# Kernel optimization log

Hardware: AMD Instinct MI355X
Metric: run time of the kernel (lower is better)

Reference implementation:

```python
import jax, jax.numpy as jnp
import numpy as np

N_NODES = 20000
N_EDGES = 320000
N_GRAPHS = 256
HIDDEN = 128
L = 4
NUM_ATOM = 28
NUM_BOND = 4
AVG_LOG = float(np.log(17.0))  # avg degree 16 -> avg_d['log']
EPS = 1e-5


def setup_inputs() -> dict:
    key = jax.random.key(0)
    ks = jax.random.split(key, 16)
    D = HIDDEN
    return {
        "x": jax.random.randint(ks[0], (N_NODES,), 0, NUM_ATOM, dtype=jnp.int32),
        "batch": jnp.sort(jax.random.randint(ks[1], (N_NODES,), 0, N_GRAPHS, dtype=jnp.int32)),
        "edge_index": jax.random.randint(ks[2], (2, N_EDGES), 0, N_NODES, dtype=jnp.int32),
        "snorm_n": jax.random.uniform(ks[3], (N_NODES, 1), dtype=jnp.float32),
        "edge_attr": jax.random.randint(ks[4], (N_EDGES,), 0, NUM_BOND, dtype=jnp.int32),
        "atom_emb": jax.random.normal(ks[5], (NUM_ATOM, D), jnp.float32) * 0.1,
        "bond_emb": jax.random.normal(ks[6], (NUM_BOND, D), jnp.float32) * 0.1,
        "pre_W": jax.random.normal(ks[7], (L, 3 * D, D), jnp.float32) / np.sqrt(3 * D),
        "pre_b": jnp.zeros((L, D), jnp.float32),
        "post_W": jax.random.normal(ks[8], (L, 13 * D, D), jnp.float32) / np.sqrt(13 * D),
        "post_b": jnp.zeros((L, D), jnp.float32),
        "mix_W": jax.random.normal(ks[9], (L, D, D), jnp.float32) / np.sqrt(D),
        "mix_b": jnp.zeros((L, D), jnp.float32),
        "bn_gamma": jnp.ones((L, D), jnp.float32),
        "bn_beta": jnp.zeros((L, D), jnp.float32),
        "r_W1": jax.random.normal(ks[10], (D, D // 2), jnp.float32) / np.sqrt(D),
        "r_b1": jnp.zeros((D // 2,), jnp.float32),
        "r_W2": jax.random.normal(ks[11], (D // 2, D // 4), jnp.float32) / np.sqrt(D // 2),
        "r_b2": jnp.zeros((D // 4,), jnp.float32),
        "r_W3": jax.random.normal(ks[12], (D // 4, 1), jnp.float32) / np.sqrt(D // 4),
        "r_b3": jnp.zeros((1,), jnp.float32),
    }


def _pna_forward(x, batch, edge_index, snorm_n, edge_attr,
                 atom_emb, bond_emb, pre_W, pre_b, post_W, post_b,
                 mix_W, mix_b, bn_gamma, bn_beta,
                 r_W1, r_b1, r_W2, r_b2, r_W3, r_b3):
    src, dst = edge_index[0], edge_index[1]
    h = atom_emb[x]                          # [N, D]
    e = bond_emb[edge_attr]                  # [E, D]
    # in-degree and PNA degree scalers (computed once)
    d = jax.ops.segment_sum(jnp.ones((src.shape[0],), h.dtype), dst, N_NODES)
    has_nb = (d > 0)[:, None]
    d_safe = jnp.maximum(d, 1.0)[:, None]
    logd = jnp.log1p(d)[:, None]
    amp = logd / AVG_LOG                     # amplification scaler
    att = AVG_LOG / jnp.maximum(logd, EPS)   # attenuation scaler
    for l in range(L):
        h_in = h
        # pretrans on edges: FC(cat(h_dst, h_src, e)) with LeakyReLU
        m = jnp.concatenate([h[dst], h[src], e], axis=-1)            # [E, 3D]
        m = jax.nn.leaky_relu(m @ pre_W[l] + pre_b[l])               # [E, D]
        # aggregators: mean, max, min, std
        mean = jax.ops.segment_sum(m, dst, N_NODES) / d_safe
        mean_sq = jax.ops.segment_sum(m * m, dst, N_NODES) / d_safe
        std = jnp.where(has_nb, jnp.sqrt(jax.nn.relu(mean_sq - mean * mean) + EPS), 0.0)
        mx = jnp.where(has_nb, jax.ops.segment_max(m, dst, N_NODES), 0.0)
        mn = jnp.where(has_nb, jax.ops.segment_min(m, dst, N_NODES), 0.0)
        agg = jnp.concatenate([mean, mx, mn, std], axis=-1)          # [N, 4D]
        agg = jnp.concatenate([agg, agg * amp, agg * att], axis=-1)  # [N, 12D]
        # posttrans FC on cat(h, agg) + mixing FC
        ph = jax.nn.leaky_relu(jnp.concatenate([h, agg], axis=-1) @ post_W[l] + post_b[l])
        ph = jax.nn.leaky_relu(ph @ mix_W[l] + mix_b[l])
        ph = ph * snorm_n                    # graph_norm
        mu = ph.mean(axis=0)                 # BatchNorm (training-mode stats)
        var = ph.var(axis=0)
        ph = bn_gamma[l] * (ph - mu) * jax.lax.rsqrt(var + EPS) + bn_beta[l]
        h = h_in + ph                        # residual
    # global mean pool per graph
    cnt = jax.ops.segment_sum(jnp.ones((x.shape[0],), h.dtype), batch, N_GRAPHS)
    g = jax.ops.segment_sum(h, batch, N_GRAPHS) / jnp.maximum(cnt, 1.0)[:, None]
    # MLPReadout: D -> D/2 -> D/4 -> 1 with ReLU
    g = jax.nn.relu(g @ r_W1 + r_b1)
    g = jax.nn.relu(g @ r_W2 + r_b2)
    return g @ r_W3 + r_b3                   # [B, 1]


def reference(x, batch, edge_index, snorm_n, edge_attr,
              atom_emb, bond_emb, pre_W, pre_b, post_W, post_b,
              mix_W, mix_b, bn_gamma, bn_beta,
              r_W1, r_b1, r_W2, r_b2, r_W3, r_b3):
    return _pna_forward(x, batch, edge_index, snorm_n, edge_attr,
                        atom_emb, bond_emb, pre_W, pre_b, post_W, post_b,
                        mix_W, mix_b, bn_gamma, bn_beta,
                        r_W1, r_b1, r_W2, r_b2, r_W3, r_b3)
```

## Files before the change

kernel.cpp:

```cpp
#include <hip/hip_runtime.h>
#include <math.h>

#define N_NODES 20000
#define N_EDGES 320000
#define N_GRAPHS 256
#define HID 128
#define NLAYERS 4
#define AVG_LOG 2.833213344056216f
#define EPS 1e-5f
#define MB64 313
#define NPAD 20032
#define SCANB 20

typedef __attribute__((ext_vector_type(8))) short short8;
typedef __attribute__((ext_vector_type(4))) float f32x4;

static __device__ __forceinline__ float leaky(float v){ return v > 0.f ? v : 0.01f*v; }

static __device__ __forceinline__ void bsplit(float f, unsigned short& hi, unsigned short& lo){
  unsigned int u = __float_as_uint(f);
  unsigned int r = u + 0x7FFFu + ((u>>16)&1u);
  hi = (unsigned short)(r>>16);
  float hf = __uint_as_float(((unsigned int)hi)<<16);
  float l = f - hf;
  unsigned int v = __float_as_uint(l);
  unsigned int s = v + 0x7FFFu + ((v>>16)&1u);
  lo = (unsigned short)(s>>16);
}

static __device__ __forceinline__ void bsplit4(float4 f, ushort4& h, ushort4& l){
  bsplit(f.x, h.x, l.x); bsplit(f.y, h.y, l.y);
  bsplit(f.z, h.z, l.z); bsplit(f.w, h.w, l.w);
}

static __device__ __forceinline__ void gload16(const void* g, void* l){
  __builtin_amdgcn_global_load_lds((const __attribute__((address_space(1))) void*)g,
                                   (__attribute__((address_space(3))) void*)l, 16, 0, 0);
}

__global__ void k_count(const int* __restrict__ dst, int* __restrict__ deg){
  int e = blockIdx.x*blockDim.x + threadIdx.x;
  if (e < N_EDGES) atomicAdd(&deg[dst[e]], 1);
}

__global__ __launch_bounds__(1024) void k_scan1(const int* __restrict__ deg,
                                                int* __restrict__ excl, int* __restrict__ btot){
  __shared__ int buf[1024];
  int b = blockIdx.x, tid = threadIdx.x;
  int i = b*1024 + tid;
  int v = (i < N_NODES) ? deg[i] : 0;
  buf[tid] = v;
  __syncthreads();
  for (int ofs = 1; ofs < 1024; ofs <<= 1){
    int t = (tid >= ofs) ? buf[tid-ofs] : 0;
    __syncthreads();
    buf[tid] += t;
    __syncthreads();
  }
  excl[i] = buf[tid] - v;
  if (tid == 1023) btot[b] = buf[1023];
}

__global__ __launch_bounds__(1024) void k_scan2(
    const int* __restrict__ deg, const int* __restrict__ excl, const int* __restrict__ btot,
    int* __restrict__ off, float* __restrict__ invd,
    float* __restrict__ amp, float* __restrict__ att){
  __shared__ int carry_s;
  int b = blockIdx.x, tid = threadIdx.x;
  if (tid == 0){
    int c = 0;
    for (int j = 0; j < b; ++j) c += btot[j];
    carry_s = c;
  }
  __syncthreads();
  int i = b*1024 + tid;
  if (i <= N_NODES){
    off[i] = carry_s + excl[i];
    if (i < N_NODES){
      float d = (float)deg[i];
      invd[i] = 1.f / fmaxf(d, 1.f);
      float ld = log1pf(d);
      amp[i] = ld / AVG_LOG;
      att[i] = AVG_LOG / fmaxf(ld, EPS);
    }
  }
}

__global__ void k_fill(const int* __restrict__ src, const int* __restrict__ dst,
                       const int* __restrict__ eattr, const int* __restrict__ off,
                       int* __restrict__ cursor,
                       int* __restrict__ srcS, int* __restrict__ eaS){
  int e = blockIdx.x*blockDim.x + threadIdx.x;
  if (e < N_EDGES){
    int d = dst[e];
    int pos = off[d] + atomicAdd(&cursor[d], 1);
    srcS[pos] = src[e]; eaS[pos] = eattr[e];
  }
}

__global__ void k_goff(const int* __restrict__ batch, int* __restrict__ goff){
  int g = threadIdx.x;
  if (g <= N_GRAPHS){
    int lo = 0, hi = N_NODES;
    while (lo < hi){ int mid = (lo+hi)>>1; if (batch[mid] < g) lo = mid+1; else hi = mid; }
    goff[g] = lo;
  }
}

__global__ void k_hinit(const int* __restrict__ x, const float* __restrict__ atom_emb,
                        float* __restrict__ h){
  int idx = blockIdx.x*blockDim.x + threadIdx.x;
  if (idx < N_NODES*32){
    int n = idx >> 5, q = idx & 31;
    ((float4*)h)[(size_t)n*32 + q] = ((const float4*)atom_emb)[(size_t)x[n]*32 + q];
  }
}

__global__ void k_bondall(const float* __restrict__ bond_emb, const float* __restrict__ pre_W,
                          const float* __restrict__ pre_b, float* __restrict__ BW3all){
  int l = blockIdx.x, tid = threadIdx.x;
  int r = tid >> 7, c = tid & 127;
  const float* W3 = pre_W + (size_t)l*384*128 + 256*128;
  float s = pre_b[l*128 + c];
  for (int k = 0; k < 128; ++k) s = fmaf(bond_emb[r*128 + k], W3[k*128 + c], s);
  BW3all[l*512 + tid] = s;
}

__global__ void k_wt(const float* __restrict__ pre_W, const float* __restrict__ post_W,
                     const float* __restrict__ mix_W,
                     unsigned short* __restrict__ whi, unsigned short* __restrict__ wlo){
  int y = blockIdx.y; int l = y/7, j = y%7;
  int K = (j>=3 && j<6) ? 512 : 128;
  const float* src; size_t off;
  if (j < 2)      { src = pre_W  + (size_t)l*384*128  + (size_t)j*128*128;            off = (size_t)j*16384; }
  else if (j == 2){ src = post_W + (size_t)l*1664*128;                                off = 2*16384; }
  else if (j < 6) { src = post_W + (size_t)l*1664*128 + (size_t)(128+(j-3)*512)*128;  off = 49152 + (size_t)(j-3)*65536; }
  else            { src = mix_W  + (size_t)l*128*128;                                 off = 245760; }
  unsigned short* dh = whi + (size_t)l*262144 + off;
  unsigned short* dl = wlo + (size_t)l*262144 + off;
  int kq8 = K/8;
  int ntask = 128*kq8;
  int t = blockIdx.x*256 + threadIdx.x;
  if (t >= ntask) return;
  int c  = t / kq8;
  int k0 = (t % kq8)*8;
  unsigned short h8[8] __attribute__((aligned(16)));
  unsigned short l8[8] __attribute__((aligned(16)));
  #pragma unroll
  for (int i=0;i<8;++i) bsplit(src[(size_t)(k0+i)*128 + c], h8[i], l8[i]);
  *(uint4*)(dh + (size_t)c*K + k0) = *(const uint4*)h8;
  *(uint4*)(dl + (size_t)c*K + k0) = *(const uint4*)l8;
}

template<int FIRST>
__global__ __launch_bounds__(256) void k_mf0(
    const unsigned short* __restrict__ whi, const unsigned short* __restrict__ wlo,
    const float* __restrict__ hin, float* __restrict__ hout,
    const float* __restrict__ tb, const double* __restrict__ bnsum,
    const float* __restrict__ gamma, const float* __restrict__ beta,
    float* __restrict__ out)
{
  const int K = 128;
  __shared__ unsigned short Ah[4*64*32], Al[4*64*32];
  __shared__ unsigned short Bh[128*32], Bl[128*32];
  __shared__ float muS[128], rsS[128], gS[128], bS[128];
  int tid = threadIdx.x, lane = tid & 63, wv = tid >> 6;
  int wm = (wv>>1)*32, wn = (wv&1)*64;
  int y = blockIdx.x % 3;
  int mbase = (blockIdx.x / 3) * 64;
  const unsigned short* wh = whi + (size_t)y*K*128;
  const unsigned short* wl = wlo + (size_t)y*K*128;
  float* outp = out + (size_t)y*(size_t)N_NODES*128;

  if (!FIRST){
    if (tid < 128){
      double mean = bnsum[tid] / (double)N_NODES;
      double var  = bnsum[128+tid] / (double)N_NODES - mean*mean;
      muS[tid] = (float)mean;
      rsS[tid] = rsqrtf((float)var + EPS);
      gS[tid]  = gamma[tid];
      bS[tid]  = beta[tid];
    }
    __syncthreads();
  }

  {
    int arow = tid >> 2, kq = tid & 3;
    int ag = mbase + arow;
    int acl = min(ag, N_NODES-1);
    float hv[32];
    const float* hp = hin + (size_t)acl*128 + kq*32;
    #pragma unroll
    for (int i=0;i<8;++i) *(float4*)&hv[i*4] = *(const float4*)(hp + i*4);
    if (!FIRST){
      const float* tp = tb + (size_t)acl*128 + kq*32;
      #pragma unroll
      for (int i=0;i<8;++i){
        float4 t4 = *(const float4*)(tp + i*4);
        int c = kq*32 + i*4;
        hv[i*4+0] += gS[c+0]*(t4.x - muS[c+0])*rsS[c+0] + bS[c+0];
        hv[i*4+1] += gS[c+1]*(t4.y - muS[c+1])*rsS[c+1] + bS[c+1];
        hv[i*4+2] += gS[c+2]*(t4.z - muS[c+2])*rsS[c+2] + bS[c+2];
        hv[i*4+3] += gS[c+3]*(t4.w - muS[c+3])*rsS[c+3] + bS[c+3];
      }
      if (y == 0 && ag < N_NODES){
        float* hw = hout + (size_t)ag*128 + kq*32;
        #pragma unroll
        for (int i=0;i<8;++i) *(float4*)(hw + i*4) = *(const float4*)&hv[i*4];
      }
    }
    int f = (arow & 3) ^ ((arow >> 2) & 3);
    unsigned short* aH = Ah + kq*2048 + arow*32;
    unsigned short* aL = Al + kq*2048 + arow*32;
    #pragma unroll
    for (int j=0;j<4;++j){
      int slot = j ^ f;
      unsigned short hh8[8] __attribute__((aligned(16)));
      unsigned short ll8[8] __attribute__((aligned(16)));
      #pragma unroll
      for (int e=0;e<8;++e) bsplit(hv[j*8+e], hh8[e], ll8[e]);
      *(uint4*)(aH + slot*8) = *(const uint4*)hh8;
      *(uint4*)(aL + slot*8) = *(const uint4*)ll8;
    }
  }

  int lq = lane >> 2, ls = lane & 3;
  int kg = ls ^ (lq & 3) ^ ((lq >> 2) & 3);
  int b_col0 = (wv*2+0)*16 + lq;
  int b_col1 = (wv*2+1)*16 + lq;
  const unsigned short* bgh0 = wh + (size_t)b_col0*K + kg*8;
  const unsigned short* bgh1 = wh + (size_t)b_col1*K + kg*8;
  const unsigned short* bgl0 = wl + (size_t)b_col0*K + kg*8;
  const unsigned short* bgl1 = wl + (size_t)b_col1*K + kg*8;
  unsigned short* b_ldsh0 = Bh + (wv*2+0)*512;
  unsigned short* b_ldsh1 = Bh + (wv*2+1)*512;
  unsigned short* b_ldsl0 = Bl + (wv*2+0)*512;
  unsigned short* b_ldsl1 = Bl + (wv*2+1)*512;

  f32x4 acc[2][4];
  #pragma unroll
  for (int mi=0;mi<2;++mi)
    #pragma unroll
    for (int ni=0;ni<4;++ni)
      acc[mi][ni] = (f32x4){0.f,0.f,0.f,0.f};

  int lr = lane & 15, lk = lane >> 4;
  int sl = lk ^ (lr & 3) ^ ((lr >> 2) & 3);

  for (int kt = 0; kt < K; kt += 32){
    gload16(bgh0 + kt, b_ldsh0);
    gload16(bgh1 + kt, b_ldsh1);
    gload16(bgl0 + kt, b_ldsl0);
    gload16(bgl1 + kt, b_ldsl1);
    __syncthreads();
    int win = kt >> 5;
    short8 ah[2], al2[2], bh4[4], bl4[4];
    #pragma unroll
    for (int mi=0;mi<2;++mi){
      int idx = win*2048 + (wm + mi*16 + lr)*32 + sl*8;
      ah[mi]  = *(const short8*)(Ah + idx);
      al2[mi] = *(const short8*)(Al + idx);
    }
    #pragma unroll
    for (int ni=0;ni<4;++ni){
      int idx = (wn + ni*16 + lr)*32 + sl*8;
      bh4[ni] = *(const short8*)(Bh + idx);
      bl4[ni] = *(const short8*)(Bl + idx);
    }
    #pragma unroll
    for (int mi=0;mi<2;++mi){
      #pragma unroll
      for (int ni=0;ni<4;++ni){
        acc[mi][ni] = __builtin_amdgcn_mfma_f32_16x16x32_bf16(ah[mi],  bh4[ni], acc[mi][ni], 0,0,0);
        acc[mi][ni] = __builtin_amdgcn_mfma_f32_16x16x32_bf16(ah[mi],  bl4[ni], acc[mi][ni], 0,0,0);
        acc[mi][ni] = __builtin_amdgcn_mfma_f32_16x16x32_bf16(al2[mi], bh4[ni], acc[mi][ni], 0,0,0);
      }
    }
    __syncthreads();
  }

  #pragma unroll
  for (int mi=0;mi<2;++mi){
    #pragma unroll
    for (int ni=0;ni<4;++ni){
      int gcol = wn + ni*16 + lr;
      #pragma unroll
      for (int r=0;r<4;++r){
        int grow = mbase + wm + mi*16 + lk*4 + r;
        if (grow < N_NODES)
          outp[(size_t)grow*128 + gcol] = acc[mi][ni][r];
      }
    }
  }
}

__global__ __launch_bounds__(256) void k_mf1(
    const unsigned short* __restrict__ whi, const unsigned short* __restrict__ wlo,
    const unsigned short* __restrict__ Ahg, const unsigned short* __restrict__ Alg,
    float* __restrict__ out)
{
  const int K = 512;
  __shared__ unsigned short Ah[64*32], Al[64*32], Bh[128*32], Bl[128*32];
  int tid = threadIdx.x;
  int lane = tid & 63;
  int wv = tid >> 6;
  int wm = (wv>>1)*32, wn = (wv&1)*64;
  int y = blockIdx.x % 3;
  int mbase = (blockIdx.x / 3) * 64;
  const unsigned short* wh = whi + (size_t)y*K*128;
  const unsigned short* wl = wlo + (size_t)y*K*128;
  int ocol = y*128;

  int lq = lane >> 2, ls = lane & 3;
  int kg = ls ^ (lq & 3) ^ ((lq >> 2) & 3);
  int a_row = wv*16 + lq;
  const unsigned short* agh = Ahg + (size_t)(mbase + a_row)*512 + kg*8;
  const unsigned short* agl = Alg + (size_t)(mbase + a_row)*512 + kg*8;
  unsigned short* a_ldsh = Ah + wv*512;
  unsigned short* a_ldsl = Al + wv*512;
  int b_col0 = (wv*2+0)*16 + lq;
  int b_col1 = (wv*2+1)*16 + lq;
  const unsigned short* bgh0 = wh + (size_t)b_col0*K + kg*8;
  const unsigned short* bgh1 = wh + (size_t)b_col1*K + kg*8;
  const unsigned short* bgl0 = wl + (size_t)b_col0*K + kg*8;
  const unsigned short* bgl1 = wl + (size_t)b_col1*K + kg*8;
  unsigned short* b_ldsh0 = Bh + (wv*2+0)*512;
  unsigned short* b_ldsh1 = Bh + (wv*2+1)*512;
  unsigned short* b_ldsl0 = Bl + (wv*2+0)*512;
  unsigned short* b_ldsl1 = Bl + (wv*2+1)*512;

  f32x4 acc[2][4];
  #pragma unroll
  for (int mi=0;mi<2;++mi)
    #pragma unroll
    for (int ni=0;ni<4;++ni)
      acc[mi][ni] = (f32x4){0.f,0.f,0.f,0.f};

  int lr = lane & 15, lk = lane >> 4;
  int sl = lk ^ (lr & 3) ^ ((lr >> 2) & 3);

  for (int kt = 0; kt < K; kt += 32){
    gload16(agh + kt, a_ldsh);
    gload16(agl + kt, a_ldsl);
    gload16(bgh0 + kt, b_ldsh0);
    gload16(bgh1 + kt, b_ldsh1);
    gload16(bgl0 + kt, b_ldsl0);
    gload16(bgl1 + kt, b_ldsl1);
    __syncthreads();
    short8 ah[2], al2[2], bh4[4], bl4[4];
    #pragma unroll
    for (int mi=0;mi<2;++mi){
      int idx = (wm + mi*16 + lr)*32 + sl*8;
      ah[mi]  = *(const short8*)(Ah + idx);
      al2[mi] = *(const short8*)(Al + idx);
    }
    #pragma unroll
    for (int ni=0;ni<4;++ni){
      int idx = (wn + ni*16 + lr)*32 + sl*8;
      bh4[ni] = *(const short8*)(Bh + idx);
      bl4[ni] = *(const short8*)(Bl + idx);
    }
    #pragma unroll
    for (int mi=0;mi<2;++mi){
      #pragma unroll
      for (int ni=0;ni<4;++ni){
        acc[mi][ni] = __builtin_amdgcn_mfma_f32_16x16x32_bf16(ah[mi],  bh4[ni], acc[mi][ni], 0,0,0);
        acc[mi][ni] = __builtin_amdgcn_mfma_f32_16x16x32_bf16(ah[mi],  bl4[ni], acc[mi][ni], 0,0,0);
        acc[mi][ni] = __builtin_amdgcn_mfma_f32_16x16x32_bf16(al2[mi], bh4[ni], acc[mi][ni], 0,0,0);
      }
    }
    __syncthreads();
  }

  #pragma unroll
  for (int mi=0;mi<2;++mi){
    #pragma unroll
    for (int ni=0;ni<4;++ni){
      int gcol = wn + ni*16 + lr;
      #pragma unroll
      for (int r=0;r<4;++r){
        int grow = mbase + wm + mi*16 + lk*4 + r;
        if (grow < N_NODES)
          out[(size_t)grow*384 + ocol + gcol] = acc[mi][ni][r];
      }
    }
  }
}

#define PITCH 40
__global__ __launch_bounds__(256) void k_mix(
    const unsigned short* __restrict__ wh, const unsigned short* __restrict__ wl,
    const float* __restrict__ Yh, const float* __restrict__ Yamt,
    const float* __restrict__ amp, const float* __restrict__ att,
    const float* __restrict__ post_b, const float* __restrict__ mix_b,
    const float* __restrict__ snorm,
    float* __restrict__ tb, double* __restrict__ bnsum)
{
  __shared__ unsigned short Ah[64*PITCH], Al[64*PITCH], Bh[128*PITCH], Bl[128*PITCH];
  __shared__ float bns[2][128], bnq[2][128];
  int tid = threadIdx.x;
  int lane = tid & 63;
  int wv = tid >> 6;
  int wm = (wv>>1)*32, wn = (wv&1)*64;
  int mbase = blockIdx.x*64;

  int a_row = tid >> 2, a_kg = tid & 3;
  int a_nrow = min(mbase + a_row, N_NODES-1);
  float av = amp[a_nrow], tv2 = att[a_nrow];
  const float* yhp = Yh   + (size_t)a_nrow*128;
  const float* yap = Yamt + (size_t)a_nrow*384;
  unsigned short* a_dh = Ah + a_row*PITCH + a_kg*8;
  unsigned short* a_dl = Al + a_row*PITCH + a_kg*8;

  f32x4 acc[2][4];
  #pragma unroll
  for (int mi=0;mi<2;++mi)
    #pragma unroll
    for (int ni=0;ni<4;++ni)
      acc[mi][ni] = (f32x4){0.f,0.f,0.f,0.f};

  int lr = lane & 15, lk = lane >> 4;

  for (int kt = 0; kt < 128; kt += 32){
    #pragma unroll
    for (int i=0;i<2;++i){
      int s = tid + 256*i;
      int col = s >> 2, kgg = s & 3;
      *(uint4*)(Bh + col*PITCH + kgg*8) = *(const uint4*)(wh + (size_t)col*128 + kt + kgg*8);
      *(uint4*)(Bl + col*PITCH + kgg*8) = *(const uint4*)(wl + (size_t)col*128 + kt + kgg*8);
    }
    {
      int c0 = kt + a_kg*8;
      float4 h0 = *(const float4*)(yhp + c0),       h1 = *(const float4*)(yhp + c0 + 4);
      float4 a0 = *(const float4*)(yap + c0),       a1 = *(const float4*)(yap + c0 + 4);
      float4 m0 = *(const float4*)(yap + 128 + c0), m1 = *(const float4*)(yap + 132 + c0);
      float4 t0 = *(const float4*)(yap + 256 + c0), t1 = *(const float4*)(yap + 260 + c0);
      float4 p0 = *(const float4*)(post_b + c0),    p1 = *(const float4*)(post_b + c0 + 4);
      float fv[8];
      fv[0] = leaky(h0.x + a0.x + av*m0.x + tv2*t0.x + p0.x);
      fv[1] = leaky(h0.y + a0.y + av*m0.y + tv2*t0.y + p0.y);
      fv[2] = leaky(h0.z + a0.z + av*m0.z + tv2*t0.z + p0.z);
      fv[3] = leaky(h0.w + a0.w + av*m0.w + tv2*t0.w + p0.w);
      fv[4] = leaky(h1.x + a1.x + av*m1.x + tv2*t1.x + p1.x);
      fv[5] = leaky(h1.y + a1.y + av*m1.y + tv2*t1.y + p1.y);
      fv[6] = leaky(h1.z + a1.z + av*m1.z + tv2*t1.z + p1.z);
      fv[7] = leaky(h1.w + a1.w + av*m1.w + tv2*t1.w + p1.w);
      unsigned short h8[8] __attribute__((aligned(16)));
      unsigned short l8[8] __attribute__((aligned(16)));
      #pragma unroll
      for (int i=0;i<8;++i) bsplit(fv[i], h8[i], l8[i]);
      *(uint4*)a_dh = *(const uint4*)h8;
      *(uint4*)a_dl = *(const uint4*)l8;
    }
    __syncthreads();
    short8 ah[2], al2[2], bh4[4], bl4[4];
    #pragma unroll
    for (int mi=0;mi<2;++mi){
      int idx = (wm + mi*16 + lr)*PITCH + lk*8;
      ah[mi]  = *(const short8*)(Ah + idx);
      al2[mi] = *(const short8*)(Al + idx);
    }
    #pragma unroll
    for (int ni=0;ni<4;++ni){
      int idx = (wn + ni*16 + lr)*PITCH + lk*8;
      bh4[ni] = *(const short8*)(Bh + idx);
      bl4[ni] = *(const short8*)(Bl + idx);
    }
    #pragma unroll
    for (int mi=0;mi<2;++mi){
      #pragma unroll
      for (int ni=0;ni<4;++ni){
        acc[mi][ni] = __builtin_amdgcn_mfma_f32_16x16x32_bf16(ah[mi],  bh4[ni], acc[mi][ni], 0,0,0);
        acc[mi][ni] = __builtin_amdgcn_mfma_f32_16x16x32_bf16(ah[mi],  bl4[ni], acc[mi][ni], 0,0,0);
        acc[mi][ni] = __builtin_amdgcn_mfma_f32_16x16x32_bf16(al2[mi], bh4[ni], acc[mi][ni], 0,0,0);
      }
    }
    __syncthreads();
  }

  float sn[2][4]; bool vld[2][4];
  #pragma unroll
  for (int mi=0;mi<2;++mi)
    #pragma unroll
    for (int r=0;r<4;++r){
      int grow = mbase + wm + mi*16 + lk*4 + r;
      vld[mi][r] = (grow < N_NODES);
      sn[mi][r] = vld[mi][r] ? snorm[grow] : 0.f;
    }
  int half = wv >> 1;
  #pragma unroll
  for (int ni=0;ni<4;++ni){
    int gcol = wn + ni*16 + lr;
    float bv = mix_b[gcol];
    float s = 0.f, q = 0.f;
    #pragma unroll
    for (int mi=0;mi<2;++mi){
      #pragma unroll
      for (int r=0;r<4;++r){
        if (vld[mi][r]){
          int grow = mbase + wm + mi*16 + lk*4 + r;
          float v = leaky(acc[mi][ni][r] + bv) * sn[mi][r];
          tb[(size_t)grow*128 + gcol] = v;
          s += v; q += v*v;
        }
      }
    }
    s += __shfl_xor(s, 16); s += __shfl_xor(s, 32);
    q += __shfl_xor(q, 16); q += __shfl_xor(q, 32);
    if (lk == 0){ bns[half][gcol] = s; bnq[half][gcol] = q; }
  }
  __syncthreads();
  if (tid < 128){
    atomicAdd(&bnsum[tid],       (double)(bns[0][tid] + bns[1][tid]));
    atomicAdd(&bnsum[128 + tid], (double)(bnq[0][tid] + bnq[1][tid]));
  }
}

__global__ __launch_bounds__(256) void k_fusedagg(
    const float* __restrict__ H1, const float* __restrict__ H2,
    const float* __restrict__ BW3,
    const int* __restrict__ srcS, const int* __restrict__ eaS,
    const int* __restrict__ off, const float* __restrict__ invd,
    unsigned short* __restrict__ aggh, unsigned short* __restrict__ aggl)
{
  __shared__ float bw[4][128];
  int tid = threadIdx.x;
  bw[tid>>7][tid&127]     = BW3[tid];
  bw[2+(tid>>7)][tid&127] = BW3[256+tid];
  __syncthreads();

  int node = blockIdx.x*8 + (tid>>5);
  int q = tid & 31;
  float4 c4 = ((const float4*)(H1 + (size_t)node*HID))[q];
  int s = off[node], e = off[node+1];
  float4 sum = make_float4(0,0,0,0), sq = make_float4(0,0,0,0);
  float4 mx = make_float4(-3.4e38f,-3.4e38f,-3.4e38f,-3.4e38f);
  float4 mn = make_float4( 3.4e38f, 3.4e38f, 3.4e38f, 3.4e38f);

  #define FA_BODY(T,B) { \
    float vx = leaky(c4.x + T.x + B.x); \
    float vy = leaky(c4.y + T.y + B.y); \
    float vz = leaky(c4.z + T.z + B.z); \
    float vw = leaky(c4.w + T.w + B.w); \
    sum.x += vx; sum.y += vy; sum.z += vz; sum.w += vw; \
    sq.x += vx*vx; sq.y += vy*vy; sq.z += vz*vz; sq.w += vw*vw; \
    mx.x = fmaxf(mx.x, vx); mx.y = fmaxf(mx.y, vy); mx.z = fmaxf(mx.z, vz); mx.w = fmaxf(mx.w, vw); \
    mn.x = fminf(mn.x, vx); mn.y = fminf(mn.y, vy); mn.z = fminf(mn.z, vz); mn.w = fminf(mn.w, vw); }

  int i = s;
  for (; i + 1 < e; i += 2){
    int sv0 = srcS[i],   ev0 = eaS[i];
    int sv1 = srcS[i+1], ev1 = eaS[i+1];
    float4 t0 = ((const float4*)(H2 + (size_t)sv0*HID))[q];
    float4 t1 = ((const float4*)(H2 + (size_t)sv1*HID))[q];
    float4 b0 = ((const float4*)(&bw[ev0][0]))[q];
    float4 b1 = ((const float4*)(&bw[ev1][0]))[q];
    FA_BODY(t0,b0)
    FA_BODY(t1,b1)
  }
  if (i < e){
    int sv = srcS[i], ev = eaS[i];
    float4 t  = ((const float4*)(H2 + (size_t)sv*HID))[q];
    float4 b4 = ((const float4*)(&bw[ev][0]))[q];
    FA_BODY(t,b4)
  }
  #undef FA_BODY

  bool has = (e > s);
  float iv = invd[node];
  float4 mean = make_float4(sum.x*iv, sum.y*iv, sum.z*iv, sum.w*iv);
  float4 msq  = make_float4(sq.x*iv,  sq.y*iv,  sq.z*iv,  sq.w*iv);
  float4 sd;
  sd.x = has ? sqrtf(fmaxf(msq.x - mean.x*mean.x, 0.f) + EPS) : 0.f;
  sd.y = has ? sqrtf(fmaxf(msq.y - mean.y*mean.y, 0.f) + EPS) : 0.f;
  sd.z = has ? sqrtf(fmaxf(msq.z - mean.z*mean.z, 0.f) + EPS) : 0.f;
  sd.w = has ? sqrtf(fmaxf(msq.w - mean.w*mean.w, 0.f) + EPS) : 0.f;
  if (!has){ mx = make_float4(0,0,0,0); mn = make_float4(0,0,0,0); }
  size_t base = (size_t)node*512 + q*4;
  ushort4 hh, ll;
  bsplit4(mean, hh, ll);
  *(ushort4*)(aggh + base      ) = hh; *(ushort4*)(aggl + base      ) = ll;
  bsplit4(mx, hh, ll);
  *(ushort4*)(aggh + base + 128) = hh; *(ushort4*)(aggl + base + 128) = ll;
  bsplit4(mn, hh, ll);
  *(ushort4*)(aggh + base + 256) = hh; *(ushort4*)(aggl + base + 256) = ll;
  bsplit4(sd, hh, ll);
  *(ushort4*)(aggh + base + 384) = hh; *(ushort4*)(aggl + base + 384) = ll;
}

__global__ __launch_bounds__(128) void k_poolread(
    const int* __restrict__ goff, const float* __restrict__ h,
    const float* __restrict__ tb, const double* __restrict__ bnsum,
    const float* __restrict__ gamma, const float* __restrict__ beta,
    const float* __restrict__ W1, const float* __restrict__ b1,
    const float* __restrict__ W2, const float* __restrict__ b2,
    const float* __restrict__ W3, const float* __restrict__ b3,
    float* __restrict__ out){
  __shared__ float gl[128];
  __shared__ float a1[64];
  __shared__ float a2[32];
  int g = blockIdx.x, tid = threadIdx.x;
  double mean = bnsum[tid] / (double)N_NODES;
  double var  = bnsum[128+tid] / (double)N_NODES - mean*mean;
  float mu = (float)mean;
  float rs = rsqrtf((float)var + EPS);
  float gm = gamma[tid], bt = beta[tid];
  int s = goff[g], e = goff[g+1];
  float sum = 0.f;
  for (int r = s; r < e; ++r){
    float v = h[(size_t)r*128 + tid] + gm*(tb[(size_t)r*128 + tid] - mu)*rs + bt;
    sum += v;
  }
  gl[tid] = sum / fmaxf((float)(e - s), 1.f);
  __syncthreads();
  if (tid < 64){
    float s1 = b1[tid];
    for (int k = 0; k < 128; ++k) s1 = fmaf(gl[k], W1[k*64 + tid], s1);
    a1[tid] = fmaxf(s1, 0.f);
  }
  __syncthreads();
  if (tid < 32){
    float s2 = b2[tid];
    for (int k = 0; k < 64; ++k) s2 = fmaf(a1[k], W2[k*32 + tid], s2);
    a2[tid] = fmaxf(s2, 0.f);
  }
  __syncthreads();
  if (tid == 0){
    float s3 = b3[0];
    for (int k = 0; k < 32; ++k) s3 = fmaf(a2[k], W3[k], s3);
    out[g] = s3;
  }
}

extern "C" void kernel_launch(void* const* d_in, const int* in_sizes, int n_in,
                              void* d_out, int out_size, void* d_ws, size_t ws_size,
                              hipStream_t stream) {
  const int*   x        = (const int*)  d_in[0];
  const int*   batch    = (const int*)  d_in[1];
  const int*   ei       = (const int*)  d_in[2];
  const float* snorm    = (const float*)d_in[3];
  const int*   eattr    = (const int*)  d_in[4];
  const float* atom_emb = (const float*)d_in[5];
  const float* bond_emb = (const float*)d_in[6];
  const float* pre_W    = (const float*)d_in[7];
  const float* pre_b    = (const float*)d_in[8];
  const float* post_W   = (const float*)d_in[9];
  const float* post_b   = (const float*)d_in[10];
  const float* mix_W    = (const float*)d_in[11];
  const float* mix_b    = (const float*)d_in[12];
  const float* bn_g     = (const float*)d_in[13];
  const float* bn_b     = (const float*)d_in[14];
  const float* rW1      = (const float*)d_in[15];
  const float* rb1      = (const float*)d_in[16];
  const float* rW2      = (const float*)d_in[17];
  const float* rb2      = (const float*)d_in[18];
  const float* rW3      = (const float*)d_in[19];
  const float* rb3      = (const float*)d_in[20];
  float* outp = (float*)d_out;

  const int* srcI = ei;
  const int* dstI = ei + N_EDGES;

  char* ws = (char*)d_ws;
  size_t o = 0;
  auto alloc = [&](size_t bytes)->char* {
    char* p = ws + o;
    o = (o + bytes + 255) & ~(size_t)255;
    return p;
  };
  int*    deg     = (int*)   alloc((size_t)N_NODES*4);
  int*    cursor  = (int*)   alloc((size_t)N_NODES*4);
  double* bnsumA  = (double*)alloc((size_t)NLAYERS*256*8);
  int*    excl    = (int*)   alloc((size_t)SCANB*1024*4);
  int*    btot    = (int*)   alloc((size_t)SCANB*4);
  int*    off     = (int*)   alloc((size_t)(N_NODES+1)*4);
  int*    goff    = (int*)   alloc((size_t)(N_GRAPHS+1)*4);
  int*    srcS    = (int*)   alloc((size_t)N_EDGES*4);
  int*    eaS     = (int*)   alloc((size_t)N_EDGES*4);
  float*  invd    = (float*) alloc((size_t)N_NODES*4);
  float*  ampb    = (float*) alloc((size_t)N_NODES*4);
  float*  attb    = (float*) alloc((size_t)N_NODES*4);
  float*  hP0     = (float*) alloc((size_t)N_NODES*HID*4);
  float*  hP1     = (float*) alloc((size_t)N_NODES*HID*4);
  float*  H3      = (float*) alloc((size_t)3*N_NODES*HID*4);
  float*  Yamt    = (float*) alloc((size_t)N_NODES*384*4);
  float*  BW3all  = (float*) alloc((size_t)NLAYERS*512*4);
  float*  tb      = (float*) alloc((size_t)N_NODES*HID*4);
  unsigned short* whi  = (unsigned short*)alloc((size_t)NLAYERS*262144*2);
  unsigned short* wlo  = (unsigned short*)alloc((size_t)NLAYERS*262144*2);
  unsigned short* aggh = (unsigned short*)alloc((size_t)NPAD*512*2);
  unsigned short* aggl = (unsigned short*)alloc((size_t)NPAD*512*2);

  hipMemsetAsync(deg, 0,
      (size_t)((char*)bnsumA - (char*)deg) + (size_t)NLAYERS*256*8, stream);
  k_count<<<(N_EDGES+255)/256, 256, 0, stream>>>(dstI, deg);
  k_scan1<<<SCANB, 1024, 0, stream>>>(deg, excl, btot);
  k_scan2<<<SCANB, 1024, 0, stream>>>(deg, excl, btot, off, invd, ampb, attb);
  k_fill<<<(N_EDGES+255)/256, 256, 0, stream>>>(srcI, dstI, eattr, off, cursor, srcS, eaS);
  k_goff<<<1, 512, 0, stream>>>(batch, goff);
  k_hinit<<<(N_NODES*32+255)/256, 256, 0, stream>>>(x, atom_emb, hP0);
  k_wt<<<dim3(32, NLAYERS*7), 256, 0, stream>>>(pre_W, post_W, mix_W, whi, wlo);
  k_bondall<<<NLAYERS, 512, 0, stream>>>(bond_emb, pre_W, pre_b, BW3all);

  float* H1 = H3;
  float* H2 = H3 + (size_t)N_NODES*HID;
  float* Yh = H3 + (size_t)2*N_NODES*HID;
  for (int l = 0; l < NLAYERS; ++l){
    const unsigned short* whl = whi + (size_t)l*262144;
    const unsigned short* wll = wlo + (size_t)l*262144;
    float* hin  = (l == 0) ? hP0 : (((l & 1) == 1) ? hP0 : hP1);
    float* hout = ((l & 1) == 1) ? hP1 : hP0;
    if (l == 0)
      k_mf0<1><<<MB64*3, 256, 0, stream>>>(whl, wll, hP0, nullptr,
          nullptr, bnsumA, bn_g, bn_b, H3);
    else
      k_mf0<0><<<MB64*3, 256, 0, stream>>>(whl, wll, hin, hout,
          tb, bnsumA + (size_t)(l-1)*256, bn_g + (size_t)(l-1)*128,
          bn_b + (size_t)(l-1)*128, H3);
    k_fusedagg<<<N_NODES/8, 256, 0, stream>>>(H1, H2, BW3all + (size_t)l*512,
        srcS, eaS, off, invd, aggh, aggl);
    k_mf1<<<MB64*3, 256, 0, stream>>>(whl + 49152, wll + 49152, aggh, aggl, Yamt);
    k_mix<<<MB64, 256, 0, stream>>>(whl + 245760, wll + 245760,
        Yh, Yamt, ampb, attb, post_b + (size_t)l*128, mix_b + (size_t)l*128,
        snorm, tb, bnsumA + (size_t)l*256);
  }

  k_poolread<<<N_GRAPHS, 128, 0, stream>>>(goff, hP1, tb,
      bnsumA + (size_t)3*256, bn_g + (size_t)3*128, bn_b + (size_t)3*128,
      rW1, rb1, rW2, rb2, rW3, rb3, outp);
}
```

Measured before the change: 555.0 us.

## Double-buffer LDS tiles in k_mf1 to overlap global loads with MFMA

The k_mf1 GEMM now keeps two LDS buffers for the A and B hi/lo tiles. It prefetches the next K-slice with direct global-to-LDS loads while the current slice is consumed by MFMAs, and it replaces the two per-iteration __syncthreads with one vmcnt wait plus barrier. The goal is to hide global load latency behind compute. LDS use doubles, which may reduce occupancy, and one kernel among many is affected.

After: 566.5 us. 2.1% more time.

```diff
diff --git a/kernel.cpp b/kernel.cpp
--- a/kernel.cpp
+++ b/kernel.cpp
@@ -300,7 +300,8 @@
     float* __restrict__ out)
 {
   const int K = 512;
-  __shared__ unsigned short Ah[64*32], Al[64*32], Bh[128*32], Bl[128*32];
+  __shared__ unsigned short Ah[2*64*32], Al[2*64*32];
+  __shared__ unsigned short Bh[2*128*32], Bl[2*128*32];
   int tid = threadIdx.x;
   int lane = tid & 63;
   int wv = tid >> 6;
@@ -316,18 +317,21 @@
   int a_row = wv*16 + lq;
   const unsigned short* agh = Ahg + (size_t)(mbase + a_row)*512 + kg*8;
   const unsigned short* agl = Alg + (size_t)(mbase + a_row)*512 + kg*8;
-  unsigned short* a_ldsh = Ah + wv*512;
-  unsigned short* a_ldsl = Al + wv*512;
   int b_col0 = (wv*2+0)*16 + lq;
   int b_col1 = (wv*2+1)*16 + lq;
   const unsigned short* bgh0 = wh + (size_t)b_col0*K + kg*8;
   const unsigned short* bgh1 = wh + (size_t)b_col1*K + kg*8;
   const unsigned short* bgl0 = wl + (size_t)b_col0*K + kg*8;
   const unsigned short* bgl1 = wl + (size_t)b_col1*K + kg*8;
-  unsigned short* b_ldsh0 = Bh + (wv*2+0)*512;
-  unsigned short* b_ldsh1 = Bh + (wv*2+1)*512;
-  unsigned short* b_ldsl0 = Bl + (wv*2+0)*512;
-  unsigned short* b_ldsl1 = Bl + (wv*2+1)*512;
+
+  auto STAGE = [&](int b, int kt){
+    gload16(agh + kt, Ah + b*2048 + wv*512);
+    gload16(agl + kt, Al + b*2048 + wv*512);
+    gload16(bgh0 + kt, Bh + b*4096 + (wv*2+0)*512);
+    gload16(bgh1 + kt, Bh + b*4096 + (wv*2+1)*512);
+    gload16(bgl0 + kt, Bl + b*4096 + (wv*2+0)*512);
+    gload16(bgl1 + kt, Bl + b*4096 + (wv*2+1)*512);
+  };
 
   f32x4 acc[2][4];
   #pragma unroll
@@ -339,24 +343,23 @@
   int lr = lane & 15, lk = lane >> 4;
   int sl = lk ^ (lr & 3) ^ ((lr >> 2) & 3);
 
+  STAGE(0, 0);
+  asm volatile("s_waitcnt vmcnt(0)" ::: "memory");
+  __builtin_amdgcn_s_barrier();
+
+  int cur = 0;
   for (int kt = 0; kt < K; kt += 32){
-    gload16(agh + kt, a_ldsh);
-    gload16(agl + kt, a_ldsl);
-    gload16(bgh0 + kt, b_ldsh0);
-    gload16(bgh1 + kt, b_ldsh1);
-    gload16(bgl0 + kt, b_ldsl0);
-    gload16(bgl1 + kt, b_ldsl1);
-    __syncthreads();
+    if (kt + 32 < K) STAGE(cur ^ 1, kt + 32);
     short8 ah[2], al2[2], bh4[4], bl4[4];
     #pragma unroll
     for (int mi=0;mi<2;++mi){
-      int idx = (wm + mi*16 + lr)*32 + sl*8;
+      int idx = cur*2048 + (wm + mi*16 + lr)*32 + sl*8;
       ah[mi]  = *(const short8*)(Ah + idx);
       al2[mi] = *(const short8*)(Al + idx);
     }
     #pragma unroll
     for (int ni=0;ni<4;++ni){
-      int idx = (wn + ni*16 + lr)*32 + sl*8;
+      int idx = cur*4096 + (wn + ni*16 + lr)*32 + sl*8;
       bh4[ni] = *(const short8*)(Bh + idx);
       bl4[ni] = *(const short8*)(Bl + idx);
     }
@@ -369,7 +372,9 @@
         acc[mi][ni] = __builtin_amdgcn_mfma_f32_16x16x32_bf16(al2[mi], bh4[ni], acc[mi][ni], 0,0,0);
       }
     }
-    __syncthreads();
+    asm volatile("s_waitcnt vmcnt(0)" ::: "memory");
+    __builtin_amdgcn_s_barrier();
+    cur ^= 1;
   }
 
   #pragma unroll
```
